# Kernel tuning notes

Hardware: AMD Instinct MI355X
Metric: run time of the kernel (lower is better)

The kernel has to match this reference:

```python
import jax, jax.numpy as jnp
import numpy as np

N = 50000          # nodes
E = 1_600_000      # edges (avg degree 32)
IN = 16            # in_node_features
H0 = 64            # hidden_features_mlp[0]
D = 32             # hidden_features_mlp[1] == hidden_features_gnn
HF = 64            # hidden_final
OUT = 3            # out_features (congestion classes)
L = 3              # gnn_layer_num
EPS = 1e-5


def gelu(x):
    return jax.nn.gelu(x, approximate=False)  # torch nn.GELU default (erf)


def bn_eval(x, g, b):
    # BatchNorm1d in eval mode with fresh running stats (mean=0, var=1)
    return x * (g / jnp.sqrt(1.0 + EPS)) + b


def ln(x, g, b):
    m = jnp.mean(x, axis=-1, keepdims=True)
    v = jnp.var(x, axis=-1, keepdims=True)
    return (x - m) / jnp.sqrt(v + EPS) * g + b


def setup_inputs() -> dict:
    key = jax.random.key(0)
    ks = jax.random.split(key, 24)
    s = 0.1
    inp = {
        "x": jax.random.normal(ks[0], (N, IN), dtype=jnp.float32),
        "edge_index": jax.random.randint(ks[1], (2, E), 0, N, dtype=jnp.int32),
        # node_emb_mlp
        "emb_W1": jax.random.normal(ks[2], (IN, H0), dtype=jnp.float32) * s,
        "emb_b1": jnp.zeros((H0,), jnp.float32),
        "emb_bn1_g": jnp.ones((H0,), jnp.float32),
        "emb_bn1_b": jnp.zeros((H0,), jnp.float32),
        "emb_W2": jax.random.normal(ks[3], (H0, D), dtype=jnp.float32) * s,
        "emb_b2": jnp.zeros((D,), jnp.float32),
        "emb_bn2_g": jnp.ones((D,), jnp.float32),
        "emb_bn2_b": jnp.zeros((D,), jnp.float32),
        # GNN layers (stacked over L)
        "msg_W": jax.random.normal(ks[4], (L, 2 * D, D), dtype=jnp.float32) * s,
        "msg_b": jnp.zeros((L, D), jnp.float32),
        "msg_ln_g": jnp.ones((L, D), jnp.float32),
        "msg_ln_b": jnp.zeros((L, D), jnp.float32),
        "upd_W": jax.random.normal(ks[5], (L, 2 * D, D), dtype=jnp.float32) * s,
        "upd_b": jnp.zeros((L, D), jnp.float32),
        "upd_ln_g": jnp.ones((L, D), jnp.float32),
        "upd_ln_b": jnp.zeros((L, D), jnp.float32),
        # final_aggregation_layer
        "fin_W1": jax.random.normal(ks[6], (D, HF), dtype=jnp.float32) * s,
        "fin_b1": jnp.zeros((HF,), jnp.float32),
        "fin_bn_g": jnp.ones((HF,), jnp.float32),
        "fin_bn_b": jnp.zeros((HF,), jnp.float32),
        "fin_W2": jax.random.normal(ks[7], (HF, OUT), dtype=jnp.float32) * s,
        "fin_b2": jnp.zeros((OUT,), jnp.float32),
    }
    return inp


def reference(x, edge_index,
              emb_W1, emb_b1, emb_bn1_g, emb_bn1_b,
              emb_W2, emb_b2, emb_bn2_g, emb_bn2_b,
              msg_W, msg_b, msg_ln_g, msg_ln_b,
              upd_W, upd_b, upd_ln_g, upd_ln_b,
              fin_W1, fin_b1, fin_bn_g, fin_bn_b, fin_W2, fin_b2):
    src = edge_index[0]  # x_j (source, messages flow source->target)
    dst = edge_index[1]  # x_i (target, aggregation index)

    # node embedding MLP (dropout = identity in eval)
    h = gelu(bn_eval(x @ emb_W1 + emb_b1, emb_bn1_g, emb_bn1_b))
    h = gelu(bn_eval(h @ emb_W2 + emb_b2, emb_bn2_g, emb_bn2_b))
    pre = h

    for l in range(L):
        x_i = h[dst]  # [E, D]
        x_j = h[src]  # [E, D]
        m = gelu(ln(jnp.concatenate([x_i, x_j], axis=-1) @ msg_W[l] + msg_b[l],
                    msg_ln_g[l], msg_ln_b[l]))                 # [E, D]
        agg = jax.ops.segment_sum(m, dst, num_segments=N)      # [N, D]
        h = h + gelu(ln(jnp.concatenate([h, agg], axis=-1) @ upd_W[l] + upd_b[l],
                        upd_ln_g[l], upd_ln_b[l]))

    h = h + pre  # residual around the GNN stack

    general_emb = h[dst] - h[src]  # node_emb_j - node_emb_i, [E, D]
    out = gelu(bn_eval(general_emb @ fin_W1 + fin_b1, fin_bn_g, fin_bn_b))
    out = out @ fin_W2 + fin_b2  # [E, OUT] cc_scores
    return out
```

## Files before the change

kernel.cpp:

```cpp
#include <hip/hip_runtime.h>

#define NN 50000
#define NE 1600000
#define FILL_B 1563
#define EMB_B  782
#define HIST_STRIDE 100096
constexpr float LN_EPS = 1e-5f;

typedef _Float16 half8 __attribute__((ext_vector_type(8)));

__device__ __forceinline__ float gelu_f(float x){
  float ax = fabsf(x) * 0.70710678118654752440f;
  float t  = __builtin_amdgcn_rcpf(fmaf(0.3275911f, ax, 1.0f));
  float e  = __expf(-ax*ax);
  float p  = t*fmaf(t, fmaf(t, fmaf(t, fmaf(t, 1.061405429f, -1.453152027f),
                                    1.421413741f), -0.284496736f), 0.254829592f);
  float er = fmaf(-p, e, 1.0f);
  return 0.5f * x * (1.0f + copysignf(er, x));
}

__device__ __forceinline__ void ld8(const float* __restrict__ p, float* r){
  float4 a=((const float4*)p)[0], b=((const float4*)p)[1];
  r[0]=a.x;r[1]=a.y;r[2]=a.z;r[3]=a.w;r[4]=b.x;r[5]=b.y;r[6]=b.z;r[7]=b.w;
}
__device__ __forceinline__ void ld16(const float* __restrict__ p, float* r){ ld8(p,r); ld8(p+8,r+8); }
__device__ __forceinline__ void st8(float* __restrict__ p, const float* r){
  float4 a,b; a.x=r[0];a.y=r[1];a.z=r[2];a.w=r[3]; b.x=r[4];b.y=r[5];b.z=r[6];b.w=r[7];
  ((float4*)p)[0]=a; ((float4*)p)[1]=b;
}

__global__ __launch_bounds__(256) void hist_kernel(const int* __restrict__ ei,
    int* __restrict__ cnt, int* __restrict__ rank){
  int t = blockIdx.x*256 + threadIdx.x;
  int i0 = t, i1 = t + HIST_STRIDE, i2 = t + 2*HIST_STRIDE, i3 = t + 3*HIST_STRIDE;
  bool v0 = i0 < NE/4, v1 = i1 < NE/4, v2 = i2 < NE/4, v3 = i3 < NE/4;
  int4 d0 = v0 ? ((const int4*)(ei + NE))[i0] : make_int4(0,0,0,0);
  int4 d1 = v1 ? ((const int4*)(ei + NE))[i1] : make_int4(0,0,0,0);
  int4 d2 = v2 ? ((const int4*)(ei + NE))[i2] : make_int4(0,0,0,0);
  int4 d3 = v3 ? ((const int4*)(ei + NE))[i3] : make_int4(0,0,0,0);
  int4 r0, r1, r2, r3;
  if(v0){ r0.x = atomicAdd(&cnt[d0.x],1); r0.y = atomicAdd(&cnt[d0.y],1);
          r0.z = atomicAdd(&cnt[d0.z],1); r0.w = atomicAdd(&cnt[d0.w],1); }
  if(v1){ r1.x = atomicAdd(&cnt[d1.x],1); r1.y = atomicAdd(&cnt[d1.y],1);
          r1.z = atomicAdd(&cnt[d1.z],1); r1.w = atomicAdd(&cnt[d1.w],1); }
  if(v2){ r2.x = atomicAdd(&cnt[d2.x],1); r2.y = atomicAdd(&cnt[d2.y],1);
          r2.z = atomicAdd(&cnt[d2.z],1); r2.w = atomicAdd(&cnt[d2.w],1); }
  if(v3){ r3.x = atomicAdd(&cnt[d3.x],1); r3.y = atomicAdd(&cnt[d3.y],1);
          r3.z = atomicAdd(&cnt[d3.z],1); r3.w = atomicAdd(&cnt[d3.w],1); }
  if(v0) ((int4*)rank)[i0] = r0;
  if(v1) ((int4*)rank)[i1] = r1;
  if(v2) ((int4*)rank)[i2] = r2;
  if(v3) ((int4*)rank)[i3] = r3;
}

#define CHUNK 52
__global__ __launch_bounds__(1024) void scan_kernel(const int* __restrict__ deg, int* __restrict__ row_ptr){
  __shared__ int sums[1024];
  int t = threadIdx.x;
  int base = t*CHUNK;
  int4 v[13];
  int ssum = 0;
  #pragma unroll
  for(int i=0;i<13;i++){
    int idx = base + 4*i;
    if(idx + 3 < NN){
      v[i] = ((const int4*)deg)[(base>>2)+i];
    } else {
      v[i].x = (idx+0<NN)?deg[idx+0]:0; v[i].y = (idx+1<NN)?deg[idx+1]:0;
      v[i].z = (idx+2<NN)?deg[idx+2]:0; v[i].w = (idx+3<NN)?deg[idx+3]:0;
    }
    ssum += v[i].x + v[i].y + v[i].z + v[i].w;
  }
  sums[t]=ssum;
  __syncthreads();
  for(int off=1; off<1024; off<<=1){
    int vv = (t>=off) ? sums[t-off] : 0;
    __syncthreads();
    sums[t] += vv;
    __syncthreads();
  }
  int run = (t>0) ? sums[t-1] : 0;
  #pragma unroll
  for(int i=0;i<13;i++){
    int idx = base + 4*i;
    int4 o;
    o.x = run; run += v[i].x;
    o.y = run; run += v[i].y;
    o.z = run; run += v[i].z;
    o.w = run; run += v[i].w;
    if(idx + 3 < NN){
      ((int4*)row_ptr)[(base>>2)+i] = o;
    } else {
      if(idx+0<NN) row_ptr[idx+0]=o.x;
      if(idx+1<NN) row_ptr[idx+1]=o.y;
      if(idx+2<NN) row_ptr[idx+2]=o.z;
      if(idx+3<NN) row_ptr[idx+3]=o.w;
    }
  }
  if(t==1023) row_ptr[NN] = sums[1023];
}

__global__ __launch_bounds__(256) void fill_kernel(const int* __restrict__ ei,
    const int* __restrict__ row_ptr, const int* __restrict__ rank, int* __restrict__ csr_src){
  int t = blockIdx.x*256 + threadIdx.x;
  if(t < NE/4){
    int4 d  = ((const int4*)(ei + NE))[t];
    int4 sv = ((const int4*)ei)[t];
    int4 rk = ((const int4*)rank)[t];
    csr_src[row_ptr[d.x] + rk.x] = sv.x;
    csr_src[row_ptr[d.y] + rk.y] = sv.y;
    csr_src[row_ptr[d.z] + rk.z] = sv.z;
    csr_src[row_ptr[d.w] + rk.w] = sv.w;
  }
}

__global__ __launch_bounds__(256) void embed_pqr_kernel(
    const float* __restrict__ x,
    const float* __restrict__ W1, const float* __restrict__ b1,
    const float* __restrict__ g1, const float* __restrict__ bb1,
    const float* __restrict__ W2, const float* __restrict__ b2,
    const float* __restrict__ g2, const float* __restrict__ bb2,
    const float* __restrict__ Wm, const float* __restrict__ bm,
    const float* __restrict__ Wu, const float* __restrict__ bu,
    const float* __restrict__ fb1, const float* __restrict__ fbng, const float* __restrict__ fbnb,
    float* __restrict__ h, float* __restrict__ pre,
    float* __restrict__ P, _Float16* __restrict__ Qh, float* __restrict__ R,
    float* __restrict__ cvec)
{
  int t = blockIdx.x*256 + threadIdx.x;
  const float rs = rsqrtf(1.0f + LN_EPS);
  if(t < 64) cvec[t] = fmaf(fb1[t], fbng[t]*rs, fbnb[t]);
  int n = t >> 2, q = t & 3;
  if(n >= NN) return;
  int base = threadIdx.x & 60;
  float4 xq = ((const float4*)x)[n*4 + q];
  float xv[16];
  #pragma unroll
  for(int m=0;m<4;m++){
    xv[4*m+0]=__shfl(xq.x, base|m);
    xv[4*m+1]=__shfl(xq.y, base|m);
    xv[4*m+2]=__shfl(xq.z, base|m);
    xv[4*m+3]=__shfl(xq.w, base|m);
  }
  float a1q[16]; ld16(b1 + q*16, a1q);
  #pragma unroll
  for(int k=0;k<16;k++){
    float w[16]; ld16(W1 + k*64 + q*16, w);
    float xk = xv[k];
    #pragma unroll
    for(int j=0;j<16;j++) a1q[j] += xk * w[j];
  }
  { float g[16], b[16]; ld16(g1+q*16,g); ld16(bb1+q*16,b);
    #pragma unroll
    for(int j=0;j<16;j++) a1q[j] = gelu_f(a1q[j]*(g[j]*rs) + b[j]); }
  float hq[8]; ld8(b2 + q*8, hq);
  #pragma unroll
  for(int m=0;m<4;m++){
    #pragma unroll
    for(int kk=0;kk<16;kk++){
      float a = __shfl(a1q[kk], base|m);
      float w[8]; ld8(W2 + (m*16+kk)*32 + q*8, w);
      #pragma unroll
      for(int j=0;j<8;j++) hq[j] += a * w[j];
    }
  }
  { float g[8], b[8]; ld8(g2+q*8,g); ld8(bb2+q*8,b);
    #pragma unroll
    for(int j=0;j<8;j++) hq[j] = gelu_f(hq[j]*(g[j]*rs) + b[j]); }
  st8(h   + (size_t)n*32 + q*8, hq);
  st8(pre + (size_t)n*32 + q*8, hq);
  float apv[8], aqv[8], arv[8];
  ld8(bm+q*8, apv); ld8(bu+q*8, arv);
  #pragma unroll
  for(int j=0;j<8;j++) aqv[j]=0.f;
  #pragma unroll
  for(int m=0;m<4;m++){
    #pragma unroll
    for(int kk=0;kk<8;kk++){
      float hk = __shfl(hq[kk], base|m);
      int k = m*8+kk;
      float wm[8],wq[8],wu[8];
      ld8(Wm + k*32      + q*8, wm);
      ld8(Wm + (32+k)*32 + q*8, wq);
      ld8(Wu + k*32      + q*8, wu);
      #pragma unroll
      for(int j=0;j<8;j++){ apv[j]+=hk*wm[j]; aqv[j]+=hk*wq[j]; arv[j]+=hk*wu[j]; }
    }
  }
  st8(P + (size_t)n*32 + q*8, apv);
  st8(R + (size_t)n*32 + q*8, arv);
  half8 qo;
  #pragma unroll
  for(int k=0;k<8;k++) qo[k] = (_Float16)aqv[k];
  *(half8*)(Qh + (size_t)n*32 + q*8) = qo;
}

__global__ __launch_bounds__(256) void msg_kernel(
    const float* __restrict__ P, const _Float16* __restrict__ Qh,
    const int* __restrict__ row_ptr, const int* __restrict__ csr_src,
    const float* __restrict__ mg, const float* __restrict__ mb,
    float* __restrict__ aggO)
{
  int tid = blockIdx.x*256 + threadIdx.x;
  int n = tid >> 4;
  int s = tid & 15;
  int slot = s >> 2;
  int q = s & 3;
  float mgq[8], mbq[8], p8[8];
  ld8(mg + q*8, mgq); ld8(mb + q*8, mbq);
  ld8(P + (size_t)n*32 + q*8, p8);
  float agg8[8] = {0,0,0,0,0,0,0,0};
  int e0 = row_ptr[n], e1 = row_ptr[n+1];
  int e = e0 + slot;
  int src = (e < e1) ? csr_src[e] : 0;
  half8 qv = *(const half8*)(Qh + (size_t)src*32 + q*8);
  while(e < e1){
    int e2 = e + 4;
    int src2 = (e2 < e1) ? csr_src[e2] : 0;
    half8 qv2 = *(const half8*)(Qh + (size_t)src2*32 + q*8);
    float v[8];
    #pragma unroll
    for(int k=0;k<8;k++) v[k] = p8[k] + (float)qv[k];
    float ps = ((v[0]+v[1])+(v[2]+v[3])) + ((v[4]+v[5])+(v[6]+v[7]));
    ps += __shfl_xor(ps,1); ps += __shfl_xor(ps,2);
    float mean = ps * 0.03125f;
    float vs = 0.f;
    #pragma unroll
    for(int k=0;k<8;k++){ float dd = v[k]-mean; vs += dd*dd; v[k]=dd; }
    vs += __shfl_xor(vs,1); vs += __shfl_xor(vs,2);
    float rstd = rsqrtf(vs*0.03125f + LN_EPS);
    #pragma unroll
    for(int k=0;k<8;k++) agg8[k] += gelu_f(v[k]*rstd*mgq[k] + mbq[k]);
    qv = qv2; e = e2;
  }
  #pragma unroll
  for(int k=0;k<8;k++) agg8[k] += __shfl_xor(agg8[k], 4);
  #pragma unroll
  for(int k=0;k<8;k++) agg8[k] += __shfl_xor(agg8[k], 8);
  if(slot==0) st8(aggO + (size_t)n*32 + q*8, agg8);
}

__global__ __launch_bounds__(256) void upd_pqr_kernel(
    const float* __restrict__ aggI, const float* __restrict__ Rio,
    const float* __restrict__ Ub,
    const float* __restrict__ ug, const float* __restrict__ ub,
    const float* __restrict__ Wm2, const float* __restrict__ bm2,
    const float* __restrict__ Wu2, const float* __restrict__ bu2,
    float* __restrict__ h,
    float* __restrict__ P, _Float16* __restrict__ Qh, float* __restrict__ Rout)
{
  int t = blockIdx.x*256 + threadIdx.x;
  int n = t >> 2, q = t & 3;
  if(n >= NN) return;
  int base = threadIdx.x & 60;
  float aggq[8], uq[8];
  ld8(aggI + (size_t)n*32 + q*8, aggq);
  ld8(Rio  + (size_t)n*32 + q*8, uq);
  #pragma unroll
  for(int m=0;m<4;m++){
    #pragma unroll
    for(int kk=0;kk<8;kk++){
      float a = __shfl(aggq[kk], base|m);
      float w[8]; ld8(Ub + (m*8+kk)*32 + q*8, w);
      #pragma unroll
      for(int j=0;j<8;j++) uq[j] += a * w[j];
    }
  }
  float sm = ((uq[0]+uq[1])+(uq[2]+uq[3])) + ((uq[4]+uq[5])+(uq[6]+uq[7]));
  sm += __shfl_xor(sm,1); sm += __shfl_xor(sm,2);
  float mean = sm * 0.03125f;
  float vs = 0.f;
  #pragma unroll
  for(int j=0;j<8;j++){ float d = uq[j]-mean; vs += d*d; uq[j]=d; }
  vs += __shfl_xor(vs,1); vs += __shfl_xor(vs,2);
  float rstd = rsqrtf(vs*0.03125f + LN_EPS);
  float ugq[8], ubq[8], hq[8];
  ld8(ug+q*8, ugq); ld8(ub+q*8, ubq);
  ld8(h + (size_t)n*32 + q*8, hq);
  #pragma unroll
  for(int j=0;j<8;j++) hq[j] += gelu_f(uq[j]*rstd*ugq[j] + ubq[j]);
  st8(h + (size_t)n*32 + q*8, hq);
  float apv[8], aqv[8], arv[8];
  ld8(bm2+q*8, apv); ld8(bu2+q*8, arv);
  #pragma unroll
  for(int j=0;j<8;j++) aqv[j]=0.f;
  #pragma unroll
  for(int m=0;m<4;m++){
    #pragma unroll
    for(int kk=0;kk<8;kk++){
      float hk = __shfl(hq[kk], base|m);
      int k = m*8+kk;
      float wm[8],wq[8],wu[8];
      ld8(Wm2 + k*32      + q*8, wm);
      ld8(Wm2 + (32+k)*32 + q*8, wq);
      ld8(Wu2 + k*32      + q*8, wu);
      #pragma unroll
      for(int j=0;j<8;j++){ apv[j]+=hk*wm[j]; aqv[j]+=hk*wq[j]; arv[j]+=hk*wu[j]; }
    }
  }
  st8(P    + (size_t)n*32 + q*8, apv);
  st8(Rout + (size_t)n*32 + q*8, arv);
  half8 qo;
  #pragma unroll
  for(int k=0;k<8;k++) qo[k] = (_Float16)aqv[k];
  *(half8*)(Qh + (size_t)n*32 + q*8) = qo;
}

__global__ __launch_bounds__(256) void upd_fin_kernel(
    const float* __restrict__ aggI, const float* __restrict__ Rio,
    const float* __restrict__ Ub,
    const float* __restrict__ ug, const float* __restrict__ ub,
    const float* __restrict__ h, const float* __restrict__ pre,
    const float* __restrict__ fW1, const float* __restrict__ fbng,
    _Float16* __restrict__ y1, _Float16* __restrict__ y2)
{
  int t = blockIdx.x*256 + threadIdx.x;
  int n = t >> 2, q = t & 3;
  if(n >= NN) return;
  int base = threadIdx.x & 60;
  const float rs = rsqrtf(1.0f + LN_EPS);
  float aggq[8], uq[8];
  ld8(aggI + (size_t)n*32 + q*8, aggq);
  ld8(Rio  + (size_t)n*32 + q*8, uq);
  #pragma unroll
  for(int m=0;m<4;m++){
    #pragma unroll
    for(int kk=0;kk<8;kk++){
      float a = __shfl(aggq[kk], base|m);
      float w[8]; ld8(Ub + (m*8+kk)*32 + q*8, w);
      #pragma unroll
      for(int j=0;j<8;j++) uq[j] += a * w[j];
    }
  }
  float sm = ((uq[0]+uq[1])+(uq[2]+uq[3])) + ((uq[4]+uq[5])+(uq[6]+uq[7]));
  sm += __shfl_xor(sm,1); sm += __shfl_xor(sm,2);
  float mean = sm * 0.03125f;
  float vs = 0.f;
  #pragma unroll
  for(int j=0;j<8;j++){ float d = uq[j]-mean; vs += d*d; uq[j]=d; }
  vs += __shfl_xor(vs,1); vs += __shfl_xor(vs,2);
  float rstd = rsqrtf(vs*0.03125f + LN_EPS);
  float ugq[8], ubq[8], hq[8], pq[8];
  ld8(ug+q*8, ugq); ld8(ub+q*8, ubq);
  ld8(h   + (size_t)n*32 + q*8, hq);
  ld8(pre + (size_t)n*32 + q*8, pq);
  #pragma unroll
  for(int j=0;j<8;j++) hq[j] += gelu_f(uq[j]*rstd*ugq[j] + ubq[j]) + pq[j];
  float acc[16];
  #pragma unroll
  for(int j=0;j<16;j++) acc[j]=0.f;
  #pragma unroll
  for(int m=0;m<4;m++){
    #pragma unroll
    for(int kk=0;kk<8;kk++){
      float hk = __shfl(hq[kk], base|m);
      float w[16]; ld16(fW1 + (m*8+kk)*64 + q*16, w);
      #pragma unroll
      for(int j=0;j<16;j++) acc[j] += hk * w[j];
    }
  }
  float fg[16]; ld16(fbng + q*16, fg);
  half8 o0, o1;
  #pragma unroll
  for(int k=0;k<8;k++){
    o0[k] = (_Float16)(acc[k]   * (fg[k]*rs));
    o1[k] = (_Float16)(acc[8+k] * (fg[8+k]*rs));
  }
  _Float16* dst = (q<2) ? (y1 + (size_t)n*32 + q*16) : (y2 + (size_t)n*32 + (q-2)*16);
  ((half8*)dst)[0] = o0; ((half8*)dst)[1] = o1;
}

__global__ __launch_bounds__(256) void finalA_kernel(
    const _Float16* __restrict__ y, const int* __restrict__ ei,
    const float* __restrict__ cvec, const float* __restrict__ W2,
    const float* __restrict__ b2, float* __restrict__ out)
{
  int t = blockIdx.x*256 + threadIdx.x;
  int e = t >> 2, q = t & 3;
  int s = __builtin_nontemporal_load(ei + e);
  int d = __builtin_nontemporal_load(ei + NE + e);
  half8 a8 = *(const half8*)(y + (size_t)d*32 + q*8);
  half8 c8 = *(const half8*)(y + (size_t)s*32 + q*8);
  float cq[8]; ld8(cvec + q*8, cq);
  float w[24]; ld8(W2+q*24, w); ld8(W2+q*24+8, w+8); ld8(W2+q*24+16, w+16);
  float o0=0.f,o1=0.f,o2=0.f;
  #pragma unroll
  for(int k=0;k<8;k++){
    float tt = gelu_f(((float)a8[k]-(float)c8[k]) + cq[k]);
    o0 += tt*w[3*k]; o1 += tt*w[3*k+1]; o2 += tt*w[3*k+2];
  }
  o0 += __shfl_xor(o0,1); o0 += __shfl_xor(o0,2);
  o1 += __shfl_xor(o1,1); o1 += __shfl_xor(o1,2);
  o2 += __shfl_xor(o2,1); o2 += __shfl_xor(o2,2);
  float ov = (q==0) ? o0 + b2[0] : (q==1) ? o1 + b2[1] : o2 + b2[2];
  if(q < 3) __builtin_nontemporal_store(ov, out + (size_t)e*3 + q);
}

__global__ __launch_bounds__(256) void finalB_kernel(
    const _Float16* __restrict__ y, const int* __restrict__ ei,
    const float* __restrict__ cvec, const float* __restrict__ W2,
    float* __restrict__ out)
{
  int t = blockIdx.x*256 + threadIdx.x;
  int e = t >> 2, q = t & 3;
  float prev = 0.f;
  if(q < 3) prev = __builtin_nontemporal_load(out + (size_t)e*3 + q);
  int s = __builtin_nontemporal_load(ei + e);
  int d = __builtin_nontemporal_load(ei + NE + e);
  half8 a8 = *(const half8*)(y + (size_t)d*32 + q*8);
  half8 c8 = *(const half8*)(y + (size_t)s*32 + q*8);
  float cq[8]; ld8(cvec + q*8, cq);
  float w[24]; ld8(W2+q*24, w); ld8(W2+q*24+8, w+8); ld8(W2+q*24+16, w+16);
  float o0=0.f,o1=0.f,o2=0.f;
  #pragma unroll
  for(int k=0;k<8;k++){
    float tt = gelu_f(((float)a8[k]-(float)c8[k]) + cq[k]);
    o0 += tt*w[3*k]; o1 += tt*w[3*k+1]; o2 += tt*w[3*k+2];
  }
  o0 += __shfl_xor(o0,1); o0 += __shfl_xor(o0,2);
  o1 += __shfl_xor(o1,1); o1 += __shfl_xor(o1,2);
  o2 += __shfl_xor(o2,1); o2 += __shfl_xor(o2,2);
  float ov = prev + ((q==0) ? o0 : (q==1) ? o1 : o2);
  if(q < 3) __builtin_nontemporal_store(ov, out + (size_t)e*3 + q);
}

extern "C" void kernel_launch(void* const* d_in, const int* in_sizes, int n_in,
                              void* d_out, int out_size, void* d_ws, size_t ws_size,
                              hipStream_t stream)
{
  (void)in_sizes; (void)n_in; (void)out_size; (void)ws_size;
  const float* x     = (const float*)d_in[0];
  const int*   ei    = (const int*)d_in[1];
  const float* eW1   = (const float*)d_in[2];
  const float* eb1   = (const float*)d_in[3];
  const float* ebn1g = (const float*)d_in[4];
  const float* ebn1b = (const float*)d_in[5];
  const float* eW2   = (const float*)d_in[6];
  const float* eb2   = (const float*)d_in[7];
  const float* ebn2g = (const float*)d_in[8];
  const float* ebn2b = (const float*)d_in[9];
  const float* msgW  = (const float*)d_in[10];
  const float* msgb  = (const float*)d_in[11];
  const float* msglng= (const float*)d_in[12];
  const float* msglnb= (const float*)d_in[13];
  const float* updW  = (const float*)d_in[14];
  const float* updb  = (const float*)d_in[15];
  const float* updlng= (const float*)d_in[16];
  const float* updlnb= (const float*)d_in[17];
  const float* fW1   = (const float*)d_in[18];
  const float* fb1   = (const float*)d_in[19];
  const float* fbng  = (const float*)d_in[20];
  const float* fbnb  = (const float*)d_in[21];
  const float* fW2   = (const float*)d_in[22];
  const float* fb2   = (const float*)d_in[23];
  float* out = (float*)d_out;

  float* f   = (float*)d_ws;
  float* h   = f;
  float* pre = f + 1*(size_t)NN*32;
  float* P   = f + 2*(size_t)NN*32;
  float* R   = f + 3*(size_t)NN*32;
  float* agg = f + 4*(size_t)NN*32;
  _Float16* Qh = (_Float16*)(f + 5*(size_t)NN*32);
  _Float16* y1 = (_Float16*)P;
  _Float16* y2 = y1 + (size_t)NN*32;
  float* cvec  = f + 5*(size_t)NN*32 + (size_t)NN*16;
  int* ip      = (int*)(cvec + 64);
  int* cnt     = ip;
  int* row_ptr = ip + NN;
  int* csr     = ip + 2*NN + 4;
  int* rank    = (int*)agg;

  hipMemsetAsync(cnt, 0, NN*sizeof(int), stream);
  hist_kernel<<<391, 256, 0, stream>>>(ei, cnt, rank);
  scan_kernel<<<1, 1024, 0, stream>>>(cnt, row_ptr);
  fill_kernel<<<FILL_B, 256, 0, stream>>>(ei, row_ptr, rank, csr);

  embed_pqr_kernel<<<EMB_B, 256, 0, stream>>>(x, eW1, eb1, ebn1g, ebn1b,
      eW2, eb2, ebn2g, ebn2b,
      msgW, msgb, updW, updb,
      fb1, fbng, fbnb,
      h, pre, P, Qh, R, cvec);

  for(int l=0; l<3; l++){
    msg_kernel<<<(NN*16)/256, 256, 0, stream>>>(P, Qh, row_ptr, csr,
        msglng + l*32, msglnb + l*32, agg);
    if(l < 2){
      upd_pqr_kernel<<<EMB_B, 256, 0, stream>>>(agg, R,
          updW + l*2048 + 1024, updlng + l*32, updlnb + l*32,
          msgW + (l+1)*2048, msgb + (l+1)*32,
          updW + (l+1)*2048, updb + (l+1)*32,
          h, P, Qh, R);
    } else {
      upd_fin_kernel<<<EMB_B, 256, 0, stream>>>(agg, R,
          updW + l*2048 + 1024, updlng + l*32, updlnb + l*32,
          h, pre, fW1, fbng, y1, y2);
    }
  }

  finalA_kernel<<<(NE*4)/256, 256, 0, stream>>>(y1, ei, cvec,      fW2,      fb2, out);
  finalB_kernel<<<(NE*4)/256, 256, 0, stream>>>(y2, ei, cvec + 32, fW2 + 96, out);
}
```

Measured before the change: 523.6 us.

## Privatize degree histogram into 8 copies and fuse CSR fill with embedding

The degree histogram is split into 8 private count arrays, chosen by block index, to spread out atomic contention. The copy index is packed into the high bits of each rank. A new reduce kernel turns the 8 copies into per-copy exclusive offsets plus total degrees before the scan. The CSR fill is merged into the embedding kernel as extra blocks, removing one launch and letting the two run concurrently, at the cost of an extra kernel, 8x larger memset, and an additional offset gather in the fill.

```diff
diff --git a/kernel.cpp b/kernel.cpp
--- a/kernel.cpp
+++ b/kernel.cpp
@@ -30,8 +30,10 @@
 }
 
 __global__ __launch_bounds__(256) void hist_kernel(const int* __restrict__ ei,
-    int* __restrict__ cnt, int* __restrict__ rank){
-  int t = blockIdx.x*256 + threadIdx.x;
+    int* __restrict__ cnt8, int* __restrict__ rank){
+  int t = blockIdx.x*256 + threadIdx.x;
+  int hi = (blockIdx.x & 7) << 20;
+  int* mycnt = cnt8 + (size_t)(blockIdx.x & 7)*NN;
   int i0 = t, i1 = t + HIST_STRIDE, i2 = t + 2*HIST_STRIDE, i3 = t + 3*HIST_STRIDE;
   bool v0 = i0 < NE/4, v1 = i1 < NE/4, v2 = i2 < NE/4, v3 = i3 < NE/4;
   int4 d0 = v0 ? ((const int4*)(ei + NE))[i0] : make_int4(0,0,0,0);
@@ -39,18 +41,34 @@
   int4 d2 = v2 ? ((const int4*)(ei + NE))[i2] : make_int4(0,0,0,0);
   int4 d3 = v3 ? ((const int4*)(ei + NE))[i3] : make_int4(0,0,0,0);
   int4 r0, r1, r2, r3;
-  if(v0){ r0.x = atomicAdd(&cnt[d0.x],1); r0.y = atomicAdd(&cnt[d0.y],1);
-          r0.z = atomicAdd(&cnt[d0.z],1); r0.w = atomicAdd(&cnt[d0.w],1); }
-  if(v1){ r1.x = atomicAdd(&cnt[d1.x],1); r1.y = atomicAdd(&cnt[d1.y],1);
-          r1.z = atomicAdd(&cnt[d1.z],1); r1.w = atomicAdd(&cnt[d1.w],1); }
-  if(v2){ r2.x = atomicAdd(&cnt[d2.x],1); r2.y = atomicAdd(&cnt[d2.y],1);
-          r2.z = atomicAdd(&cnt[d2.z],1); r2.w = atomicAdd(&cnt[d2.w],1); }
-  if(v3){ r3.x = atomicAdd(&cnt[d3.x],1); r3.y = atomicAdd(&cnt[d3.y],1);
-          r3.z = atomicAdd(&cnt[d3.z],1); r3.w = atomicAdd(&cnt[d3.w],1); }
+  if(v0){ r0.x = hi|atomicAdd(&mycnt[d0.x],1); r0.y = hi|atomicAdd(&mycnt[d0.y],1);
+          r0.z = hi|atomicAdd(&mycnt[d0.z],1); r0.w = hi|atomicAdd(&mycnt[d0.w],1); }
+  if(v1){ r1.x = hi|atomicAdd(&mycnt[d1.x],1); r1.y = hi|atomicAdd(&mycnt[d1.y],1);
+          r1.z = hi|atomicAdd(&mycnt[d1.z],1); r1.w = hi|atomicAdd(&mycnt[d1.w],1); }
+  if(v2){ r2.x = hi|atomicAdd(&mycnt[d2.x],1); r2.y = hi|atomicAdd(&mycnt[d2.y],1);
+          r2.z = hi|atomicAdd(&mycnt[d2.z],1); r2.w = hi|atomicAdd(&mycnt[d2.w],1); }
+  if(v3){ r3.x = hi|atomicAdd(&mycnt[d3.x],1); r3.y = hi|atomicAdd(&mycnt[d3.y],1);
+          r3.z = hi|atomicAdd(&mycnt[d3.z],1); r3.w = hi|atomicAdd(&mycnt[d3.w],1); }
   if(v0) ((int4*)rank)[i0] = r0;
   if(v1) ((int4*)rank)[i1] = r1;
   if(v2) ((int4*)rank)[i2] = r2;
   if(v3) ((int4*)rank)[i3] = r3;
+}
+
+__global__ __launch_bounds__(256) void reduce8_kernel(int* __restrict__ cnt8,
+    int* __restrict__ deg){
+  int t = blockIdx.x*256 + threadIdx.x;
+  if(t >= NN/4) return;
+  int4 c[8];
+  #pragma unroll
+  for(int x=0;x<8;x++) c[x] = ((const int4*)(cnt8 + (size_t)x*NN))[t];
+  int4 run = make_int4(0,0,0,0);
+  #pragma unroll
+  for(int x=0;x<8;x++){
+    ((int4*)(cnt8 + (size_t)x*NN))[t] = run;
+    run.x += c[x].x; run.y += c[x].y; run.z += c[x].z; run.w += c[x].w;
+  }
+  ((int4*)deg)[t] = run;
 }
 
 #define CHUNK 52
@@ -100,21 +118,10 @@
   if(t==1023) row_ptr[NN] = sums[1023];
 }
 
-__global__ __launch_bounds__(256) void fill_kernel(const int* __restrict__ ei,
-    const int* __restrict__ row_ptr, const int* __restrict__ rank, int* __restrict__ csr_src){
-  int t = blockIdx.x*256 + threadIdx.x;
-  if(t < NE/4){
-    int4 d  = ((const int4*)(ei + NE))[t];
-    int4 sv = ((const int4*)ei)[t];
-    int4 rk = ((const int4*)rank)[t];
-    csr_src[row_ptr[d.x] + rk.x] = sv.x;
-    csr_src[row_ptr[d.y] + rk.y] = sv.y;
-    csr_src[row_ptr[d.z] + rk.z] = sv.z;
-    csr_src[row_ptr[d.w] + rk.w] = sv.w;
-  }
-}
-
-__global__ __launch_bounds__(256) void embed_pqr_kernel(
+__global__ __launch_bounds__(256) void fill_embed_kernel(
+    const int* __restrict__ ei, const int* __restrict__ row_ptr,
+    const int* __restrict__ rank, const int* __restrict__ offs8,
+    int* __restrict__ csr,
     const float* __restrict__ x,
     const float* __restrict__ W1, const float* __restrict__ b1,
     const float* __restrict__ g1, const float* __restrict__ bb1,
@@ -127,6 +134,19 @@
     float* __restrict__ P, _Float16* __restrict__ Qh, float* __restrict__ R,
     float* __restrict__ cvec)
 {
+  if(blockIdx.x >= EMB_B){
+    int t = (blockIdx.x - EMB_B)*256 + threadIdx.x;
+    if(t < NE/4){
+      int4 d  = ((const int4*)(ei + NE))[t];
+      int4 sv = ((const int4*)ei)[t];
+      int4 rk = ((const int4*)rank)[t];
+      csr[row_ptr[d.x] + offs8[(size_t)((unsigned)rk.x>>20)*NN + d.x] + (rk.x & 0xFFFFF)] = sv.x;
+      csr[row_ptr[d.y] + offs8[(size_t)((unsigned)rk.y>>20)*NN + d.y] + (rk.y & 0xFFFFF)] = sv.y;
+      csr[row_ptr[d.z] + offs8[(size_t)((unsigned)rk.z>>20)*NN + d.z] + (rk.z & 0xFFFFF)] = sv.z;
+      csr[row_ptr[d.w] + offs8[(size_t)((unsigned)rk.w>>20)*NN + d.w] + (rk.w & 0xFFFFF)] = sv.w;
+    }
+    return;
+  }
   int t = blockIdx.x*256 + threadIdx.x;
   const float rs = rsqrtf(1.0f + LN_EPS);
   if(t < 64) cvec[t] = fmaf(fb1[t], fbng[t]*rs, fbnb[t]);
@@ -466,17 +486,18 @@
   _Float16* y2 = y1 + (size_t)NN*32;
   float* cvec  = f + 5*(size_t)NN*32 + (size_t)NN*16;
   int* ip      = (int*)(cvec + 64);
-  int* cnt     = ip;
-  int* row_ptr = ip + NN;
-  int* csr     = ip + 2*NN + 4;
+  int* cnt8    = ip;
+  int* deg     = ip + 8*NN;
+  int* row_ptr = ip + 9*NN;
+  int* csr     = ip + 10*NN + 4;
   int* rank    = (int*)agg;
 
-  hipMemsetAsync(cnt, 0, NN*sizeof(int), stream);
-  hist_kernel<<<391, 256, 0, stream>>>(ei, cnt, rank);
-  scan_kernel<<<1, 1024, 0, stream>>>(cnt, row_ptr);
-  fill_kernel<<<FILL_B, 256, 0, stream>>>(ei, row_ptr, rank, csr);
-
-  embed_pqr_kernel<<<EMB_B, 256, 0, stream>>>(x, eW1, eb1, ebn1g, ebn1b,
+  hipMemsetAsync(cnt8, 0, (size_t)8*NN*sizeof(int), stream);
+  hist_kernel<<<391, 256, 0, stream>>>(ei, cnt8, rank);
+  reduce8_kernel<<<(NN/4+255)/256, 256, 0, stream>>>(cnt8, deg);
+  scan_kernel<<<1, 1024, 0, stream>>>(deg, row_ptr);
+  fill_embed_kernel<<<EMB_B + FILL_B, 256, 0, stream>>>(ei, row_ptr, rank, cnt8, csr,
+      x, eW1, eb1, ebn1g, ebn1b,
       eW2, eb2, ebn2g, ebn2b,
       msgW, msgb, updW, updb,
       fb1, fbng, fbnb,
```

Result: faster. 500.6 us (-4.4%).
